# Optimization experiments

Hardware: AMD Instinct MI355X
Metric: run time of the kernel (lower is better)

Reference implementation:

```python
import jax, jax.numpy as jnp
import numpy as np

B, S, E, H = 8, 1024, 512, 16
L = S            # block_len == seq_len (only valid operating point of the module)
D = E // H       # d_head = 32


def setup_inputs() -> dict:
    key = jax.random.key(0)
    k0, k1, k2, k3, k4 = jax.random.split(key, 5)
    scale = 1.0 / np.sqrt(E).astype(np.float32)
    return {
        "x": jax.random.normal(k0, (B, S, E), dtype=jnp.float32),
        "Wq": jax.random.normal(k1, (E, E), dtype=jnp.float32) * scale,  # torch Linear weight (out,in)
        "Wk": jax.random.normal(k2, (E, E), dtype=jnp.float32) * scale,
        "Wv": jax.random.normal(k3, (E, E), dtype=jnp.float32) * scale,
        "Er": jax.random.normal(k4, (2 * L - 1, D), dtype=jnp.float32),  # relative pos embeddings
    }


def reference(x, Wq, Wk, Wv, Er):
    b, s, e = x.shape
    l = s  # block_len == seq_len -> pad_len = 0, n_block = 1
    # projections (torch Linear: y = x @ W.T), split heads -> [b, h, l, d]
    q = (x @ Wq.T).reshape(b, s, H, D).transpose(0, 2, 1, 3)
    k = (x @ Wk.T).reshape(b, s, H, D).transpose(0, 2, 1, 3)
    v = (x @ Wv.T).reshape(b, s, H, D).transpose(0, 2, 1, 3)

    # content scores [b, h, l, l]
    QK = jnp.einsum('bhqd,bhkd->bhqk', q, k)

    # relative position bias. The pad/flatten/reshape skew trick in the original
    # is exactly Srel[i, j] = q[i] . Er[j - i + L - 1] (mask_QEr zeros entries
    # that the skew never reads). Implemented as a gather of Er + einsum.
    rel_idx = jnp.arange(l)[None, :] - jnp.arange(l)[:, None] + (l - 1)  # [l, l] in [0, 2l-2]
    Er_g = Er[rel_idx]                                                   # [l, l, d]
    Srel = jnp.einsum('bhid,ijd->bhij', q, Er_g)

    # NOTE: the module's causal `mask` buffer is never applied in forward.
    attn = jax.nn.softmax((QK + Srel) / np.sqrt(D).astype(np.float32), axis=-1)
    out = jnp.einsum('bhij,bhjd->bhid', attn, v)       # [b, h, l, d]
    out = out.transpose(0, 2, 1, 3).reshape(b, s, e)   # merge heads
    return out  # dropout is identity in eval / p=0
```

## Files before the change

### kernel.cpp

```cpp
#include <hip/hip_runtime.h>
#include <hip/hip_bf16.h>


typedef short bf16x8 __attribute__((ext_vector_type(8)));
typedef float f32x4 __attribute__((ext_vector_type(4)));
typedef unsigned int u32x2 __attribute__((ext_vector_type(2)));
typedef unsigned int u32x4 __attribute__((ext_vector_type(4)));

#if __has_builtin(__builtin_amdgcn_exp2f)
#define EXP2F(x) __builtin_amdgcn_exp2f(x)
#else
#define EXP2F(x) exp2f(x)
#endif

constexpr int Bb = 8, Ss = 1024, Ee = 512, Hh = 16, Dd = 32;
#define QSCALE 0.25503486f

__device__ __forceinline__ bf16x8 ldg_frag(const __hip_bfloat16* p) {
    return *reinterpret_cast<const bf16x8*>(p);
}

__device__ __forceinline__ unsigned pack_bf16(float lo, float hi) {
    unsigned r;
    asm("v_cvt_pk_bf16_f32 %0, %1, %2" : "=v"(r) : "v"(lo), "v"(hi));
    return r;
}

__device__ __forceinline__ float bperm_f(int addr, float v) {
    return __builtin_bit_cast(float,
        __builtin_amdgcn_ds_bpermute(addr, __builtin_bit_cast(int, v)));
}

__device__ __forceinline__ void stage16(const void* g, void* l) {
    typedef const __attribute__((address_space(1))) char gch;
    typedef __attribute__((address_space(3))) char lch;
    __builtin_amdgcn_global_load_lds((gch*)g, (lch*)l, 16, 0, 0);
}

__global__ __launch_bounds__(256) void convert_kernel(
    const float* __restrict__ x,  const float* __restrict__ wq,
    const float* __restrict__ wk, const float* __restrict__ wv,
    const float* __restrict__ er,
    __hip_bfloat16* __restrict__ xb, __hip_bfloat16* __restrict__ wb,
    __hip_bfloat16* __restrict__ erb)
{
    const int GX = 1048576, GW = 65536, GE = 16376;
    int g = blockIdx.x * 256 + threadIdx.x;
    if (g >= GX + 3 * GW + GE) return;
    const float* src;
    __hip_bfloat16* dst;
    int rel;
    if (g < GX)               { src = x;  dst = xb;          rel = g; }
    else if (g < GX +   GW)   { src = wq; dst = wb;          rel = g - GX; }
    else if (g < GX + 2*GW)   { src = wk; dst = wb + 262144; rel = g - GX - GW; }
    else if (g < GX + 3*GW)   { src = wv; dst = wb + 524288; rel = g - GX - 2*GW; }
    else                      { src = er; dst = erb;         rel = g - GX - 3*GW; }
    const float4 v = *reinterpret_cast<const float4*>(src + (size_t)rel * 4);
    u32x2 pk;
    pk[0] = pack_bf16(v.x, v.y);
    pk[1] = pack_bf16(v.z, v.w);
    *reinterpret_cast<u32x2*>(dst + (size_t)rel * 4) = pk;
}

__global__ __launch_bounds__(256) void proj_kernel(
    const __hip_bfloat16* __restrict__ xb,
    const __hip_bfloat16* __restrict__ wb,
    __hip_bfloat16* __restrict__ Qs,
    __hip_bfloat16* __restrict__ Kh,
    unsigned* __restrict__ Vt32)
{
    const int tid  = threadIdx.x;
    const int wave = tid >> 6;
    const int lane = tid & 63;
    const int li   = lane & 15;
    const int quad = lane >> 4;

    const int m0    = blockIdx.y * 64;
    const int nbase = blockIdx.x * 256 + wave * 64;

    __shared__ __align__(16) char smem[20480];

    f32x4 acc[4][4];
    #pragma unroll
    for (int rf = 0; rf < 4; ++rf)
        #pragma unroll
        for (int t = 0; t < 4; ++t) acc[rf][t] = f32x4{0.f, 0.f, 0.f, 0.f};

    const int srow   = lane >> 2;
    const int schunk = ((lane & 3) ^ ((lane >> 3) & 3)) << 4;
    const char* Asrc = (const char*)xb
        + (((size_t)(m0 + wave * 16 + srow)) << 10) + schunk;
    const char* Bsrc = (const char*)wb
        + (((size_t)(blockIdx.x * 256 + wave * 64 + srow)) << 10) + schunk;
    char* Adst = smem + wave * 1024;
    char* Bdst = smem + 4096 + wave * 4096;

    const int rchunk = (quad ^ ((li >> 1) & 3)) << 4;

    for (int k0 = 0; k0 < Ee; k0 += 32) {
        const int kb = k0 * 2;
        stage16(Asrc + kb,         Adst);
        stage16(Bsrc + kb,         Bdst);
        stage16(Bsrc + kb + 16384, Bdst + 1024);
        stage16(Bsrc + kb + 32768, Bdst + 2048);
        stage16(Bsrc + kb + 49152, Bdst + 3072);
        __syncthreads();

        bf16x8 a[4], bfr[4];
        #pragma unroll
        for (int rf = 0; rf < 4; ++rf)
            a[rf] = *reinterpret_cast<const bf16x8*>(
                smem + (rf * 16 + li) * 64 + rchunk);
        #pragma unroll
        for (int t = 0; t < 4; ++t)
            bfr[t] = *reinterpret_cast<const bf16x8*>(
                smem + 4096 + (wave * 64 + t * 16 + li) * 64 + rchunk);
        #pragma unroll
        for (int rf = 0; rf < 4; ++rf)
            #pragma unroll
            for (int t = 0; t < 4; ++t)
                acc[rf][t] = __builtin_amdgcn_mfma_f32_16x16x32_bf16(
                    a[rf], bfr[t], acc[rf][t], 0, 0, 0);
        __syncthreads();
    }

    const int mat = nbase >> 9;
    const int nn0 = nbase & 511;
    const int bb  = m0 >> 10;
    const int sb  = m0 & 1023;
    if (mat == 2) {
        #pragma unroll
        for (int t = 0; t < 4; ++t) {
            int nn = nn0 + t * 16 + li;
            int h = nn >> 5, d = nn & 31;
            size_t base = ((size_t)(bb * Hh + h) * Dd + d) * 512
                        + (sb >> 5) * 16 + quad * 4;
            #pragma unroll
            for (int p = 0; p < 2; ++p) {
                u32x4 pk;
                #pragma unroll
                for (int r = 0; r < 4; ++r)
                    pk[r] = pack_bf16(acc[2*p][t][r], acc[2*p+1][t][r]);
                *reinterpret_cast<u32x4*>(Vt32 + base + (size_t)p * 16) = pk;
            }
        }
    } else {
        __hip_bfloat16* dst = (mat == 0) ? Qs : Kh;
        const float sc = (mat == 0) ? QSCALE : 1.0f;
        #pragma unroll
        for (int rf = 0; rf < 4; ++rf) {
            const int srw = sb + rf * 16 + quad * 4;
            #pragma unroll
            for (int t = 0; t < 4; ++t) {
                int nn = nn0 + t * 16 + li;
                int h = nn >> 5, d = nn & 31;
                size_t base = ((size_t)(bb * Hh + h) * Ss + srw) * Dd + d;
                #pragma unroll
                for (int r = 0; r < 4; r += 2) {
                    unsigned w = pack_bf16(acc[rf][t][r]     * sc,
                                           acc[rf][t][r + 1] * sc);
                    dst[base + (size_t)r * Dd] =
                        __builtin_bit_cast(__hip_bfloat16, (unsigned short)(w & 0xffffu));
                    dst[base + (size_t)(r + 1) * Dd] =
                        __builtin_bit_cast(__hip_bfloat16, (unsigned short)(w >> 16));
                }
            }
        }
    }
}

__global__ __launch_bounds__(256) void attn_kernel(
    const __hip_bfloat16* __restrict__ Qs,
    const __hip_bfloat16* __restrict__ Kh,
    const __hip_bfloat16* __restrict__ Vt,
    const __hip_bfloat16* __restrict__ Er,
    float* __restrict__ out)
{
    const int tid  = threadIdx.x;
    const int wave = tid >> 6;
    const int lane = tid & 63;
    const int li   = lane & 15;
    const int quad = lane >> 4;

    const int c  = blockIdx.x & 127;
    const int b  = c >> 4;
    const int h  = c & 15;
    const int ib = blockIdx.x >> 7;
    const int i0 = ib * 128 + wave * 32;

    const __hip_bfloat16* Qp  = Qs + (size_t)(b * Hh + h) * Ss * Dd;
    const __hip_bfloat16* Kp  = Kh + (size_t)(b * Hh + h) * Ss * Dd;
    const unsigned*       Vp32 = reinterpret_cast<const unsigned*>(Vt)
                               + (size_t)(b * Hh + h) * Dd * 512;

    __shared__ unsigned pb_lds[4][4][16 * 20];
    __shared__ __align__(16) unsigned char kvbuf[8192];
    unsigned* pbA0 = pb_lds[wave][0];
    unsigned* pbA1 = pb_lds[wave][1];
    unsigned* pbB0 = pb_lds[wave][2];
    unsigned* pbB1 = pb_lds[wave][3];

    const bf16x8 qfA = ldg_frag(Qp + (i0      + li) * Dd + quad * 8);
    const bf16x8 qfB = ldg_frag(Qp + (i0 + 16 + li) * Dd + quad * 8);

    int addr4[4];
    bool sel[4];
    #pragma unroll
    for (int r = 0; r < 4; ++r) {
        const int row = quad * 4 + r;
        addr4[r] = (16 * quad + ((li - row + 15) & 15)) * 4;
        sel[r]   = (li + row >= 15);
    }
    const int pbw = quad * 80 + li;
    const int pbr = li * 20 + quad * 4;

    const int krow  = wave * 16 + (lane >> 2);
    const int kcol8 = ((lane & 3) ^ ((lane >> 3) & 3)) * 8;
    char* kdst = (char*)kvbuf + wave * 1024;
    const int vrow = wave * 8 + (lane >> 3);
    const int vcol4 = 4 * ((lane & 7) ^ ((lane >> 3) & 7));
    char* vdst = (char*)kvbuf + 4096 + wave * 1024;
    const int swz = (li & 7) << 4;
    const int kr  = (quad ^ ((li >> 1) & 3)) << 4;

    f32x4 oA0 = f32x4{0,0,0,0}, oA1 = f32x4{0,0,0,0};
    f32x4 oB0 = f32x4{0,0,0,0}, oB1 = f32x4{0,0,0,0};
    f32x4 lsA = f32x4{0,0,0,0}, lsB = f32x4{0,0,0,0};
    const f32x4 zero = f32x4{0,0,0,0};

    bf16x8 ones;
    #pragma unroll
    for (int i = 0; i < 8; ++i) ones[i] = (short)0x3F80;

    const int rb0 = 1008 - i0;
    bf16x8 em = ldg_frag(Er + (rb0 - 16 + li) * Dd + quad * 8);
    bf16x8 e0 = ldg_frag(Er + (rb0      + li) * Dd + quad * 8);

    for (int j0 = 0; j0 < Ss; j0 += 64) {
        stage16(Kp + (size_t)(j0 + krow) * Dd + kcol8, kdst);
        stage16(Vp32 + (size_t)vrow * 512 + (j0 >> 1) + vcol4, vdst);

        const int rb = j0 - i0 + 1008;
        bf16x8 e1 = ldg_frag(Er + (rb + 16 + li) * Dd + quad * 8);
        bf16x8 e2 = ldg_frag(Er + (rb + 32 + li) * Dd + quad * 8);
        bf16x8 e3 = ldg_frag(Er + (rb + 48 + li) * Dd + quad * 8);
        bf16x8 e4 = ldg_frag(Er + (rb + 64 + li) * Dd + quad * 8);

        __syncthreads();

        const char* Kb = (const char*)kvbuf;
        const char* Vb = (const char*)kvbuf + 4096;
        bf16x8 k0 = *reinterpret_cast<const bf16x8*>(Kb + (     li) * 64 + kr);
        bf16x8 k1 = *reinterpret_cast<const bf16x8*>(Kb + (16 + li) * 64 + kr);
        bf16x8 k2 = *reinterpret_cast<const bf16x8*>(Kb + (32 + li) * 64 + kr);
        bf16x8 k3 = *reinterpret_cast<const bf16x8*>(Kb + (48 + li) * 64 + kr);
        bf16x8 v0 = *reinterpret_cast<const bf16x8*>(Vb + (     li) * 128 + ((     quad * 16) ^ swz));
        bf16x8 v1 = *reinterpret_cast<const bf16x8*>(Vb + (16 + li) * 128 + ((     quad * 16) ^ swz));
        bf16x8 v2 = *reinterpret_cast<const bf16x8*>(Vb + (     li) * 128 + ((64 + quad * 16) ^ swz));
        bf16x8 v3 = *reinterpret_cast<const bf16x8*>(Vb + (16 + li) * 128 + ((64 + quad * 16) ^ swz));

        {
            __builtin_amdgcn_s_setprio(1);
            f32x4 s0 = __builtin_amdgcn_mfma_f32_16x16x32_bf16(qfA, k0, zero, 0, 0, 0);
            f32x4 s1 = __builtin_amdgcn_mfma_f32_16x16x32_bf16(qfA, k1, zero, 0, 0, 0);
            f32x4 s2 = __builtin_amdgcn_mfma_f32_16x16x32_bf16(qfA, k2, zero, 0, 0, 0);
            f32x4 s3 = __builtin_amdgcn_mfma_f32_16x16x32_bf16(qfA, k3, zero, 0, 0, 0);
            f32x4 q0 = __builtin_amdgcn_mfma_f32_16x16x32_bf16(qfA, e0, zero, 0, 0, 0);
            f32x4 q1 = __builtin_amdgcn_mfma_f32_16x16x32_bf16(qfA, e1, zero, 0, 0, 0);
            f32x4 q2 = __builtin_amdgcn_mfma_f32_16x16x32_bf16(qfA, e2, zero, 0, 0, 0);
            f32x4 q3 = __builtin_amdgcn_mfma_f32_16x16x32_bf16(qfA, e3, zero, 0, 0, 0);
            f32x4 q4 = __builtin_amdgcn_mfma_f32_16x16x32_bf16(qfA, e4, zero, 0, 0, 0);
            __builtin_amdgcn_s_setprio(0);
            float p0[4], p1[4], p2[4], p3[4];
            #pragma unroll
            for (int r = 0; r < 4; ++r) {
                float m0 = sel[r] ? q0[r] : q1[r];
                float m1 = sel[r] ? q1[r] : q2[r];
                float m2 = sel[r] ? q2[r] : q3[r];
                float m3 = sel[r] ? q3[r] : q4[r];
                p0[r] = EXP2F(s0[r] + bperm_f(addr4[r], m0));
                p1[r] = EXP2F(s1[r] + bperm_f(addr4[r], m1));
                p2[r] = EXP2F(s2[r] + bperm_f(addr4[r], m2));
                p3[r] = EXP2F(s3[r] + bperm_f(addr4[r], m3));
            }
            #pragma unroll
            for (int r = 0; r < 4; ++r) {
                pbA0[pbw + 20 * r] = pack_bf16(p0[r], p1[r]);
                pbA1[pbw + 20 * r] = pack_bf16(p2[r], p3[r]);
            }
            bf16x8 pf0 = *reinterpret_cast<const bf16x8*>(&pbA0[pbr]);
            bf16x8 pf1 = *reinterpret_cast<const bf16x8*>(&pbA1[pbr]);
            __builtin_amdgcn_s_setprio(1);
            oA0 = __builtin_amdgcn_mfma_f32_16x16x32_bf16(pf0, v0, oA0, 0, 0, 0);
            oA1 = __builtin_amdgcn_mfma_f32_16x16x32_bf16(pf0, v1, oA1, 0, 0, 0);
            oA0 = __builtin_amdgcn_mfma_f32_16x16x32_bf16(pf1, v2, oA0, 0, 0, 0);
            oA1 = __builtin_amdgcn_mfma_f32_16x16x32_bf16(pf1, v3, oA1, 0, 0, 0);
            lsA = __builtin_amdgcn_mfma_f32_16x16x32_bf16(pf0, ones, lsA, 0, 0, 0);
            lsA = __builtin_amdgcn_mfma_f32_16x16x32_bf16(pf1, ones, lsA, 0, 0, 0);
            __builtin_amdgcn_s_setprio(0);
        }

        {
            __builtin_amdgcn_s_setprio(1);
            f32x4 s0 = __builtin_amdgcn_mfma_f32_16x16x32_bf16(qfB, k0, zero, 0, 0, 0);
            f32x4 s1 = __builtin_amdgcn_mfma_f32_16x16x32_bf16(qfB, k1, zero, 0, 0, 0);
            f32x4 s2 = __builtin_amdgcn_mfma_f32_16x16x32_bf16(qfB, k2, zero, 0, 0, 0);
            f32x4 s3 = __builtin_amdgcn_mfma_f32_16x16x32_bf16(qfB, k3, zero, 0, 0, 0);
            f32x4 q0 = __builtin_amdgcn_mfma_f32_16x16x32_bf16(qfB, em, zero, 0, 0, 0);
            f32x4 q1 = __builtin_amdgcn_mfma_f32_16x16x32_bf16(qfB, e0, zero, 0, 0, 0);
            f32x4 q2 = __builtin_amdgcn_mfma_f32_16x16x32_bf16(qfB, e1, zero, 0, 0, 0);
            f32x4 q3 = __builtin_amdgcn_mfma_f32_16x16x32_bf16(qfB, e2, zero, 0, 0, 0);
            f32x4 q4 = __builtin_amdgcn_mfma_f32_16x16x32_bf16(qfB, e3, zero, 0, 0, 0);
            __builtin_amdgcn_s_setprio(0);
            float p0[4], p1[4], p2[4], p3[4];
            #pragma unroll
            for (int r = 0; r < 4; ++r) {
                float m0 = sel[r] ? q0[r] : q1[r];
                float m1 = sel[r] ? q1[r] : q2[r];
                float m2 = sel[r] ? q2[r] : q3[r];
                float m3 = sel[r] ? q3[r] : q4[r];
                p0[r] = EXP2F(s0[r] + bperm_f(addr4[r], m0));
                p1[r] = EXP2F(s1[r] + bperm_f(addr4[r], m1));
                p2[r] = EXP2F(s2[r] + bperm_f(addr4[r], m2));
                p3[r] = EXP2F(s3[r] + bperm_f(addr4[r], m3));
            }
            #pragma unroll
            for (int r = 0; r < 4; ++r) {
                pbB0[pbw + 20 * r] = pack_bf16(p0[r], p1[r]);
                pbB1[pbw + 20 * r] = pack_bf16(p2[r], p3[r]);
            }
            bf16x8 pf0 = *reinterpret_cast<const bf16x8*>(&pbB0[pbr]);
            bf16x8 pf1 = *reinterpret_cast<const bf16x8*>(&pbB1[pbr]);
            __builtin_amdgcn_s_setprio(1);
            oB0 = __builtin_amdgcn_mfma_f32_16x16x32_bf16(pf0, v0, oB0, 0, 0, 0);
            oB1 = __builtin_amdgcn_mfma_f32_16x16x32_bf16(pf0, v1, oB1, 0, 0, 0);
            oB0 = __builtin_amdgcn_mfma_f32_16x16x32_bf16(pf1, v2, oB0, 0, 0, 0);
            oB1 = __builtin_amdgcn_mfma_f32_16x16x32_bf16(pf1, v3, oB1, 0, 0, 0);
            lsB = __builtin_amdgcn_mfma_f32_16x16x32_bf16(pf0, ones, lsB, 0, 0, 0);
            lsB = __builtin_amdgcn_mfma_f32_16x16x32_bf16(pf1, ones, lsB, 0, 0, 0);
            __builtin_amdgcn_s_setprio(0);
        }

        em = e3;
        e0 = e4;
        __syncthreads();
    }

    #pragma unroll
    for (int r = 0; r < 4; ++r) {
        lsA[r] = 1.0f / lsA[r];
        lsB[r] = 1.0f / lsB[r];
    }
    #pragma unroll
    for (int r = 0; r < 4; ++r) {
        const int srowA = i0 + quad * 4 + r;
        float* opA = out + ((size_t)b * Ss + srowA) * Ee + h * Dd;
        opA[li]      = oA0[r] * lsA[r];
        opA[16 + li] = oA1[r] * lsA[r];
        float* opB = opA + 16 * Ee;
        opB[li]      = oB0[r] * lsB[r];
        opB[16 + li] = oB1[r] * lsB[r];
    }
}

extern "C" void kernel_launch(void* const* d_in, const int* in_sizes, int n_in,
                              void* d_out, int out_size, void* d_ws, size_t ws_size,
                              hipStream_t stream) {
    const float* x  = (const float*)d_in[0];
    const float* Wq = (const float*)d_in[1];
    const float* Wk = (const float*)d_in[2];
    const float* Wv = (const float*)d_in[3];
    const float* Er = (const float*)d_in[4];
    float* out = (float*)d_out;

    __hip_bfloat16* xb  = reinterpret_cast<__hip_bfloat16*>(d_ws);
    __hip_bfloat16* wbb = xb  + (size_t)8192 * 512;
    __hip_bfloat16* erb = wbb + (size_t)1536 * 512;
    __hip_bfloat16* Qs  = erb + 65536;
    __hip_bfloat16* Kh  = Qs  + (size_t)Bb * Hh * Ss * Dd;
    __hip_bfloat16* Vt  = Kh  + (size_t)Bb * Hh * Ss * Dd;

    convert_kernel<<<4929, 256, 0, stream>>>(x, Wq, Wk, Wv, Er, xb, wbb, erb);
    proj_kernel<<<dim3(6, 128), 256, 0, stream>>>(
        xb, wbb, Qs, Kh, reinterpret_cast<unsigned*>(Vt));
    attn_kernel<<<dim3(1024), 256, 0, stream>>>(Qs, Kh, Vt, erb, out);
}
```

Measured before the change: 166.8 us.

## Double-buffer LDS staging in projection and attention kernels

```diff
diff --git a/kernel.cpp b/kernel.cpp
--- a/kernel.cpp
+++ b/kernel.cpp
@@ -78,7 +78,7 @@
     const int m0    = blockIdx.y * 64;
     const int nbase = blockIdx.x * 256 + wave * 64;
 
-    __shared__ __align__(16) char smem[20480];
+    __shared__ __align__(16) char smem[2][20480];
 
     f32x4 acc[4][4];
     #pragma unroll
@@ -92,36 +92,56 @@
         + (((size_t)(m0 + wave * 16 + srow)) << 10) + schunk;
     const char* Bsrc = (const char*)wb
         + (((size_t)(blockIdx.x * 256 + wave * 64 + srow)) << 10) + schunk;
-    char* Adst = smem + wave * 1024;
-    char* Bdst = smem + 4096 + wave * 4096;
 
     const int rchunk = (quad ^ ((li >> 1) & 3)) << 4;
 
+    {
+        char* N = smem[0];
+        stage16(Asrc,         N + wave * 1024);
+        stage16(Bsrc,         N + 4096 + wave * 4096);
+        stage16(Bsrc + 16384, N + 4096 + wave * 4096 + 1024);
+        stage16(Bsrc + 32768, N + 4096 + wave * 4096 + 2048);
+        stage16(Bsrc + 49152, N + 4096 + wave * 4096 + 3072);
+        asm volatile("" ::: "memory");
+    }
+
+    int cur = 0;
     for (int k0 = 0; k0 < Ee; k0 += 32) {
-        const int kb = k0 * 2;
-        stage16(Asrc + kb,         Adst);
-        stage16(Bsrc + kb,         Bdst);
-        stage16(Bsrc + kb + 16384, Bdst + 1024);
-        stage16(Bsrc + kb + 32768, Bdst + 2048);
-        stage16(Bsrc + kb + 49152, Bdst + 3072);
-        __syncthreads();
-
+        __builtin_amdgcn_sched_barrier(0);
+        asm volatile("s_waitcnt vmcnt(0)" ::: "memory");
+        __builtin_amdgcn_s_barrier();
+        asm volatile("" ::: "memory");
+        __builtin_amdgcn_sched_barrier(0);
+
+        const char* S = smem[cur];
         bf16x8 a[4], bfr[4];
         #pragma unroll
         for (int rf = 0; rf < 4; ++rf)
             a[rf] = *reinterpret_cast<const bf16x8*>(
-                smem + (rf * 16 + li) * 64 + rchunk);
+                S + (rf * 16 + li) * 64 + rchunk);
         #pragma unroll
         for (int t = 0; t < 4; ++t)
             bfr[t] = *reinterpret_cast<const bf16x8*>(
-                smem + 4096 + (wave * 64 + t * 16 + li) * 64 + rchunk);
+                S + 4096 + (wave * 64 + t * 16 + li) * 64 + rchunk);
+
+        {
+            const int kb = ((k0 + 32) & 511) * 2;
+            char* N = smem[cur ^ 1];
+            stage16(Asrc + kb,         N + wave * 1024);
+            stage16(Bsrc + kb,         N + 4096 + wave * 4096);
+            stage16(Bsrc + kb + 16384, N + 4096 + wave * 4096 + 1024);
+            stage16(Bsrc + kb + 32768, N + 4096 + wave * 4096 + 2048);
+            stage16(Bsrc + kb + 49152, N + 4096 + wave * 4096 + 3072);
+            asm volatile("" ::: "memory");
+        }
+
         #pragma unroll
         for (int rf = 0; rf < 4; ++rf)
             #pragma unroll
             for (int t = 0; t < 4; ++t)
                 acc[rf][t] = __builtin_amdgcn_mfma_f32_16x16x32_bf16(
                     a[rf], bfr[t], acc[rf][t], 0, 0, 0);
-        __syncthreads();
+        cur ^= 1;
     }
 
     const int mat = nbase >> 9;
@@ -194,11 +214,23 @@
                                + (size_t)(b * Hh + h) * Dd * 512;
 
     __shared__ unsigned pb_lds[4][4][16 * 20];
-    __shared__ __align__(16) unsigned char kvbuf[8192];
+    __shared__ __align__(16) unsigned char kvbuf[2][8192];
     unsigned* pbA0 = pb_lds[wave][0];
     unsigned* pbA1 = pb_lds[wave][1];
     unsigned* pbB0 = pb_lds[wave][2];
     unsigned* pbB1 = pb_lds[wave][3];
+
+    const int krow  = wave * 16 + (lane >> 2);
+    const int kcol8 = ((lane & 3) ^ ((lane >> 3) & 3)) * 8;
+    const int vrow = wave * 8 + (lane >> 3);
+    const int vcol4 = 4 * ((lane & 7) ^ ((lane >> 3) & 7));
+    const int swz = (li & 7) << 4;
+    const int kr  = (quad ^ ((li >> 1) & 3)) << 4;
+
+    stage16(Kp + (size_t)krow * Dd + kcol8, (char*)kvbuf[0] + wave * 1024);
+    stage16(Vp32 + (size_t)vrow * 512 + vcol4,
+            (char*)kvbuf[0] + 4096 + wave * 1024);
+    asm volatile("" ::: "memory");
 
     const bf16x8 qfA = ldg_frag(Qp + (i0      + li) * Dd + quad * 8);
     const bf16x8 qfB = ldg_frag(Qp + (i0 + 16 + li) * Dd + quad * 8);
@@ -214,15 +246,6 @@
     const int pbw = quad * 80 + li;
     const int pbr = li * 20 + quad * 4;
 
-    const int krow  = wave * 16 + (lane >> 2);
-    const int kcol8 = ((lane & 3) ^ ((lane >> 3) & 3)) * 8;
-    char* kdst = (char*)kvbuf + wave * 1024;
-    const int vrow = wave * 8 + (lane >> 3);
-    const int vcol4 = 4 * ((lane & 7) ^ ((lane >> 3) & 7));
-    char* vdst = (char*)kvbuf + 4096 + wave * 1024;
-    const int swz = (li & 7) << 4;
-    const int kr  = (quad ^ ((li >> 1) & 3)) << 4;
-
     f32x4 oA0 = f32x4{0,0,0,0}, oA1 = f32x4{0,0,0,0};
     f32x4 oB0 = f32x4{0,0,0,0}, oB1 = f32x4{0,0,0,0};
     f32x4 lsA = f32x4{0,0,0,0}, lsB = f32x4{0,0,0,0};
@@ -236,20 +259,22 @@
     bf16x8 em = ldg_frag(Er + (rb0 - 16 + li) * Dd + quad * 8);
     bf16x8 e0 = ldg_frag(Er + (rb0      + li) * Dd + quad * 8);
 
+    int cur = 0;
     for (int j0 = 0; j0 < Ss; j0 += 64) {
-        stage16(Kp + (size_t)(j0 + krow) * Dd + kcol8, kdst);
-        stage16(Vp32 + (size_t)vrow * 512 + (j0 >> 1) + vcol4, vdst);
-
         const int rb = j0 - i0 + 1008;
         bf16x8 e1 = ldg_frag(Er + (rb + 16 + li) * Dd + quad * 8);
         bf16x8 e2 = ldg_frag(Er + (rb + 32 + li) * Dd + quad * 8);
         bf16x8 e3 = ldg_frag(Er + (rb + 48 + li) * Dd + quad * 8);
         bf16x8 e4 = ldg_frag(Er + (rb + 64 + li) * Dd + quad * 8);
 
-        __syncthreads();
-
-        const char* Kb = (const char*)kvbuf;
-        const char* Vb = (const char*)kvbuf + 4096;
+        __builtin_amdgcn_sched_barrier(0);
+        asm volatile("s_waitcnt vmcnt(4)" ::: "memory");
+        __builtin_amdgcn_s_barrier();
+        asm volatile("" ::: "memory");
+        __builtin_amdgcn_sched_barrier(0);
+
+        const char* Kb = (const char*)kvbuf[cur];
+        const char* Vb = Kb + 4096;
         bf16x8 k0 = *reinterpret_cast<const bf16x8*>(Kb + (     li) * 64 + kr);
         bf16x8 k1 = *reinterpret_cast<const bf16x8*>(Kb + (16 + li) * 64 + kr);
         bf16x8 k2 = *reinterpret_cast<const bf16x8*>(Kb + (32 + li) * 64 + kr);
@@ -258,6 +283,15 @@
         bf16x8 v1 = *reinterpret_cast<const bf16x8*>(Vb + (16 + li) * 128 + ((     quad * 16) ^ swz));
         bf16x8 v2 = *reinterpret_cast<const bf16x8*>(Vb + (     li) * 128 + ((64 + quad * 16) ^ swz));
         bf16x8 v3 = *reinterpret_cast<const bf16x8*>(Vb + (16 + li) * 128 + ((64 + quad * 16) ^ swz));
+
+        {
+            const int jn = (j0 + 64) & 1023;
+            char* N = (char*)kvbuf[cur ^ 1];
+            stage16(Kp + (size_t)(jn + krow) * Dd + kcol8, N + wave * 1024);
+            stage16(Vp32 + (size_t)vrow * 512 + (jn >> 1) + vcol4,
+                    N + 4096 + wave * 1024);
+            asm volatile("" ::: "memory");
+        }
 
         {
             __builtin_amdgcn_s_setprio(1);
@@ -343,7 +377,7 @@
 
         em = e3;
         e0 = e4;
-        __syncthreads();
+        cur ^= 1;
     }
 
     #pragma unroll
```

New measurement: 162.9 us (median of 2 runs). -2.4%, faster.
